# Performance work log

Hardware: AMD Instinct MI355X
Metric: run time of the kernel (lower is better)

Reference implementation:

```python
import jax, jax.numpy as jnp
import numpy as np

L, HID, H, D = 2, 128, 8, 16  # layers, hidden, heads, head_dim
N, E = 50000, 800000
CLAMP = 5.0
BN_SCALE = 1.0 / np.sqrt(1.0 + 1e-5)  # eval BN with running mean 0, var 1


def signed_sqrt(s):
    # sqrt(relu(s)) - sqrt(relu(-s)), with safe gradients at 0
    pos = jnp.sqrt(jnp.where(s > 0, s, 1.0))
    neg = jnp.sqrt(jnp.where(s < 0, -s, 1.0))
    return jnp.where(s > 0, pos, 0.0) - jnp.where(s < 0, neg, 0.0)


def setup_inputs() -> dict:
    key = jax.random.key(0)
    ks = jax.random.split(key, 32)
    sc = 0.05
    inp = {
        "x": jax.random.normal(ks[0], (N, HID), jnp.float32),
        "edge_index": jax.random.randint(ks[1], (2, E), 0, N, jnp.int64)
        if jax.config.jax_enable_x64 else jax.random.randint(ks[1], (2, E), 0, N, jnp.int32),
        "edge_attr": jax.random.normal(ks[2], (E, HID), jnp.float32),
        "Wq": jax.random.normal(ks[3], (L, HID, HID), jnp.float32) * sc,
        "bq": jnp.zeros((L, HID), jnp.float32),
        "Wk": jax.random.normal(ks[4], (L, HID, HID), jnp.float32) * sc,
        "Wv": jax.random.normal(ks[5], (L, HID, HID), jnp.float32) * sc,
        "We": jax.random.normal(ks[6], (L, HID, 2 * HID), jnp.float32) * sc,
        "be": jnp.zeros((L, 2 * HID), jnp.float32),
        "Aw": jax.random.normal(ks[7], (L, D, H, 1), jnp.float32) * 0.2,
        "VeRow": jax.random.normal(ks[8], (L, D, H, D), jnp.float32) * sc,
        "Woh": jax.random.normal(ks[9], (L, HID, HID), jnp.float32) * sc,
        "boh": jnp.zeros((L, HID), jnp.float32),
        "Woe": jax.random.normal(ks[10], (L, HID, HID), jnp.float32) * sc,
        "boe": jnp.zeros((L, HID), jnp.float32),
        "deg_coef": jax.random.normal(ks[11], (L, 1, HID, 2), jnp.float32) * 0.2,
        "W1": jax.random.normal(ks[12], (L, HID, 2 * HID), jnp.float32) * sc,
        "b1": jnp.zeros((L, 2 * HID), jnp.float32),
        "W2": jax.random.normal(ks[13], (L, 2 * HID, HID), jnp.float32) * sc,
        "b2": jnp.zeros((L, HID), jnp.float32),
    }
    return inp


def _forward(x, edge_attr, edge_index, Wq, bq, Wk, Wv, We, be, Aw, VeRow,
             Woh, boh, Woe, boe, deg_coef, W1, b1, W2, b2):
    src, dst = edge_index[0], edge_index[1]
    n = x.shape[0]
    deg = jax.ops.segment_sum(jnp.ones_like(dst, jnp.float32), dst, num_segments=n)
    log_deg = jnp.log(deg + 1.0)[:, None]  # [N,1]

    for l in range(L):
        Qh = (x @ Wq[l] + bq[l]).reshape(n, H, D)
        Kh = (x @ Wk[l]).reshape(n, H, D)
        Vh = (x @ Wv[l]).reshape(n, H, D)
        Ep = (edge_attr @ We[l] + be[l]).reshape(-1, H, 2 * D)
        E_w, E_b = Ep[:, :, :D], Ep[:, :, D:]

        s = (Kh[src] + Qh[dst]) * E_w           # [E,H,D]
        s = signed_sqrt(s) + E_b
        e_t = jax.nn.relu(s)                     # [E,H,D]
        wE = e_t.reshape(-1, H * D)

        sc = jnp.einsum('ehd,dhc->ehc', e_t, Aw[l])   # [E,H,1]
        sc = jnp.clip(sc, -CLAMP, CLAMP)
        m = jax.ops.segment_max(sc, dst, num_segments=n)
        a = jnp.exp(sc - m[dst])
        denom = jax.ops.segment_sum(a, dst, num_segments=n)[dst] + 1e-16
        attn = a / denom                          # [E,H,1]

        wV = jax.ops.segment_sum(Vh[src] * attn, dst, num_segments=n)   # [N,H,D]
        rowV = jax.ops.segment_sum(e_t * attn, dst, num_segments=n)     # [N,H,D]
        wV = wV + jnp.einsum('nhd,dhc->nhc', rowV, VeRow[l])

        h = wV.reshape(n, H * D)
        h = h * deg_coef[l, :, :, 0] + (h * log_deg) * deg_coef[l, :, :, 1]
        h = h @ Woh[l] + boh[l]
        e = wE @ Woe[l] + boe[l]
        h = (x + h) * BN_SCALE
        e = (edge_attr + e) * BN_SCALE
        h2 = jax.nn.relu(h @ W1[l] + b1[l]) @ W2[l] + b2[l]
        h = (h + h2) * BN_SCALE
        x, edge_attr = h, e
    return x, edge_attr


def reference(x, edge_index, edge_attr, Wq, bq, Wk, Wv, We, be, Aw, VeRow,
              Woh, boh, Woe, boe, deg_coef, W1, b1, W2, b2):
    return _forward(x, edge_attr, edge_index, Wq, bq, Wk, Wv, We, be, Aw, VeRow,
                    Woh, boh, Woe, boe, deg_coef, W1, b1, W2, b2)
```

## Files before the change

kernel.cpp:

```cpp
#include <hip/hip_runtime.h>

#define NN 50000
#define NE 800000
#define CLAMPV 5.0f
#define BNS 0.9999950000374997f
#define EPKS 132
#define NBLK 49

typedef __attribute__((ext_vector_type(8))) short s16x8;
typedef __attribute__((ext_vector_type(8))) __bf16 bf16x8;
typedef __attribute__((ext_vector_type(4))) float f32x4;

__device__ inline f32x4 mfma16(s16x8 a, s16x8 b, f32x4 c) {
    return __builtin_amdgcn_mfma_f32_16x16x32_bf16(
        __builtin_bit_cast(bf16x8, a), __builtin_bit_cast(bf16x8, b), c, 0, 0, 0);
}

__device__ inline unsigned short bf16r(float f) {
    return __builtin_bit_cast(unsigned short, (__bf16)f);
}

__device__ inline int pk2(float a, float b) {
    return (int)(unsigned)bf16r(a) | ((int)(unsigned)bf16r(b) << 16);
}

__device__ inline float b2f(unsigned short u) {
    return __builtin_bit_cast(float, (unsigned)u << 16);
}


__global__ __launch_bounds__(256) void k_deg(const int* __restrict__ ei, int* __restrict__ deg) {
    int e = blockIdx.x * 256 + threadIdx.x;
    if (e < NE) atomicAdd(&deg[ei[NE + e]], 1);
}

__global__ __launch_bounds__(1024) void k_scan1(const int* __restrict__ deg, int* __restrict__ offs,
                                                int* __restrict__ bsum, float* __restrict__ logdeg) {
    __shared__ int sm[1024];
    int i = blockIdx.x * 1024 + threadIdx.x;
    int v = (i < NN) ? deg[i] : 0;
    if (i < NN) logdeg[i] = logf((float)v + 1.0f);
    sm[threadIdx.x] = v;
    __syncthreads();
    for (int s = 1; s < 1024; s <<= 1) {
        int t = (threadIdx.x >= s) ? sm[threadIdx.x - s] : 0;
        __syncthreads();
        sm[threadIdx.x] += t;
        __syncthreads();
    }
    if (i < NN) offs[i + 1] = sm[threadIdx.x];
    if (threadIdx.x == 1023) bsum[blockIdx.x] = sm[1023];
    if (blockIdx.x == 0 && threadIdx.x == 0) offs[0] = 0;
}

__global__ void k_scan2(int* __restrict__ bsum) {
    if (threadIdx.x == 0) {
        int acc = 0;
        for (int i = 0; i < NBLK; ++i) { int v = bsum[i]; bsum[i] = acc; acc += v; }
    }
}

__global__ __launch_bounds__(1024) void k_scan3(int* __restrict__ offs, const int* __restrict__ bsum) {
    int i = blockIdx.x * 1024 + threadIdx.x;
    if (i < NN) offs[i + 1] += bsum[blockIdx.x];
}

__global__ __launch_bounds__(256) void k_fill(const int* __restrict__ ei, const int* __restrict__ offs,
                                              int* __restrict__ cursor, int* __restrict__ csr_src,
                                              int* __restrict__ epos) {
    int e = blockIdx.x * 256 + threadIdx.x;
    if (e < NE) {
        int d = ei[NE + e];
        int pos = offs[d] + atomicAdd(&cursor[d], 1);
        csr_src[pos] = ei[e];
        epos[e] = pos;
    }
}

#define PL_A (128*256)
#define PL_B (128*128)
__global__ __launch_bounds__(256) void k_packAll(
    const float* __restrict__ We,  const float* __restrict__ Woe, const float* __restrict__ Wq,
    const float* __restrict__ Wk,  const float* __restrict__ Wv,  const float* __restrict__ Woh,
    const float* __restrict__ W1,  const float* __restrict__ W2,  const float* __restrict__ VR,
    short* __restrict__ Wep,  short* __restrict__ Woep, short* __restrict__ Wqp,
    short* __restrict__ Wkp,  short* __restrict__ Wvp,  short* __restrict__ Wohp,
    short* __restrict__ W1p,  short* __restrict__ W2p,  short* __restrict__ VRp) {
    int s = blockIdx.x * 256 + threadIdx.x;
    const float* W; short* out; int ncol, perL; bool vr = false;
    if (s < 2 * PL_A) { W = We; out = Wep; ncol = 256; perL = PL_A; }
    else if ((s -= 2 * PL_A) < 2 * PL_B) { W = Woe; out = Woep; ncol = 128; perL = PL_B; }
    else if ((s -= 2 * PL_B) < 2 * PL_B) { W = Wq;  out = Wqp;  ncol = 128; perL = PL_B; }
    else if ((s -= 2 * PL_B) < 2 * PL_B) { W = Wk;  out = Wkp;  ncol = 128; perL = PL_B; }
    else if ((s -= 2 * PL_B) < 2 * PL_B) { W = Wv;  out = Wvp;  ncol = 128; perL = PL_B; }
    else if ((s -= 2 * PL_B) < 2 * PL_B) { W = Woh; out = Wohp; ncol = 128; perL = PL_B; }
    else if ((s -= 2 * PL_B) < 2 * PL_A) { W = W1;  out = W1p;  ncol = 256; perL = PL_A; }
    else if ((s -= 2 * PL_A) < 2 * PL_A) { W = W2;  out = W2p;  ncol = 128; perL = PL_A; }
    else if ((s -= 2 * PL_A) < 2 * PL_B) { W = VR;  out = VRp;  ncol = 128; perL = PL_B; vr = true; }
    else return;
    int l = s / perL, q = s % perL;
    int j = q & 7; int t2 = q >> 3; int kg = t2 & 3; t2 >>= 2;
    int col = t2 % ncol; int kt = t2 / ncol;
    int k = kt * 32 + kg * 8 + j;
    float v;
    if (vr) v = ((k >> 4) == (col >> 4)) ? VR[l * 2048 + (k & 15) * 128 + col] : 0.f;
    else    v = W[(size_t)l * perL + k * ncol + col];
    out[(size_t)l * perL + q] = (short)bf16r(v);
}


__global__ __launch_bounds__(512) void k_qkv(const float* __restrict__ x,
                                             const short* __restrict__ Wqp, const float* __restrict__ bq,
                                             const short* __restrict__ Wkp, const short* __restrict__ Wvp,
                                             unsigned short* __restrict__ Qh, unsigned short* __restrict__ Kh,
                                             unsigned short* __restrict__ Vh) {
    __shared__ short xsw[64 * 128];
    int t = threadIdx.x;
    int ci = t & 15, r0 = t >> 4;
    int n0 = blockIdx.x * 64;
    for (int rr = r0; rr < 64; rr += 32) {
        int n = n0 + rr;
        int4 pkv = make_int4(0, 0, 0, 0);
        if (n < NN) {
            const float4* src = (const float4*)(x + (size_t)n * 128 + ci * 8);
            float4 v0 = src[0], v1 = src[1];
            pkv.x = pk2(v0.x, v0.y); pkv.y = pk2(v0.z, v0.w);
            pkv.z = pk2(v1.x, v1.y); pkv.w = pk2(v1.z, v1.w);
        }
        int byte = (rr * 256 + ci * 16) ^ ((rr & 7) << 4);
        *(int4*)((char*)xsw + byte) = pkv;
    }
    __syncthreads();
    int lane = t & 63, w = t >> 6;
    int l15 = lane & 15, kg = lane >> 4;
    f32x4 acc[4][3];
#pragma unroll
    for (int m = 0; m < 4; ++m)
#pragma unroll
        for (int q = 0; q < 3; ++q) { acc[m][q][0] = 0.f; acc[m][q][1] = 0.f; acc[m][q][2] = 0.f; acc[m][q][3] = 0.f; }
    int col = w * 16 + l15;
#pragma unroll
    for (int kt = 0; kt < 4; ++kt) {
        s16x8 a[4];
#pragma unroll
        for (int m = 0; m < 4; ++m) {
            int row = m * 16 + l15;
            int abyte = (row * 256 + kt * 64 + kg * 16) ^ ((l15 & 7) << 4);
            a[m] = *(const s16x8*)((const char*)xsw + abyte);
        }
        size_t bo = ((size_t)((kt * 128 + col) * 4 + kg)) * 8;
        s16x8 bqf = *(const s16x8*)(Wqp + bo);
        s16x8 bkf = *(const s16x8*)(Wkp + bo);
        s16x8 bvf = *(const s16x8*)(Wvp + bo);
#pragma unroll
        for (int m = 0; m < 4; ++m) {
            acc[m][0] = mfma16(a[m], bqf, acc[m][0]);
            acc[m][1] = mfma16(a[m], bkf, acc[m][1]);
            acc[m][2] = mfma16(a[m], bvf, acc[m][2]);
        }
    }
    float bqv = bq[col];
#pragma unroll
    for (int m = 0; m < 4; ++m)
#pragma unroll
        for (int i = 0; i < 4; ++i) {
            int n = n0 + m * 16 + kg * 4 + i;
            if (n < NN) {
                Qh[(size_t)n * 128 + col] = bf16r(acc[m][0][i] + bqv);
                Kh[(size_t)n * 128 + col] = bf16r(acc[m][1][i]);
                Vh[(size_t)n * 128 + col] = bf16r(acc[m][2][i]);
            }
        }
}

template<bool IN_F32>
__global__ __launch_bounds__(512) void k_edgeA(const void* __restrict__ ea_, const int* __restrict__ ei,
                                               const int* __restrict__ epos,
                                               const short* __restrict__ Wep, const float* __restrict__ be,
                                               const float* __restrict__ Aw,
                                               const unsigned short* __restrict__ Qh,
                                               const unsigned short* __restrict__ Kh,
                                               unsigned short* __restrict__ e_t, float* __restrict__ sc,
                                               const short* __restrict__ Woep, const float* __restrict__ boe,
                                               void* __restrict__ eout_) {
    __shared__ short eas[64 * 128];
    __shared__ int epts[64 * EPKS];
    const float* eaf = (const float*)ea_;
    const unsigned short* eab = (const unsigned short*)ea_;
    unsigned short* eout_b = (unsigned short*)eout_;
    float* eout_f = (float*)eout_;

    int e0 = blockIdx.x * 64;
    int t = threadIdx.x;
    int ci = t & 15, r0 = t >> 4;
    int eA = e0 + r0, eB = eA + 32;
    int siA = ei[eA], diA = ei[NE + eA], posA = epos[eA];
    int siB = ei[eB], diB = ei[NE + eB], posB = epos[eB];

    {
#pragma unroll
        for (int h = 0; h < 2; ++h) {
            int rr = r0 + h * 32;
            int4 pkv;
            if (IN_F32) {
                const float4* src = (const float4*)(eaf + (size_t)(e0 + rr) * 128 + ci * 8);
                float4 v0 = src[0], v1 = src[1];
                pkv.x = pk2(v0.x, v0.y); pkv.y = pk2(v0.z, v0.w);
                pkv.z = pk2(v1.x, v1.y); pkv.w = pk2(v1.z, v1.w);
            } else {
                pkv = *(const int4*)(eab + (size_t)(e0 + rr) * 128 + ci * 8);
            }
            int byte = (rr * 256 + ci * 16) ^ ((rr & 7) << 4);
            *(int4*)((char*)eas + byte) = pkv;
        }
    }
    __syncthreads();
    union { int4 v; unsigned short us[8]; } kuA, quA, kuB, quB;
    kuA.v = *(const int4*)(Kh + (size_t)siA * 128 + ci * 8);
    quA.v = *(const int4*)(Qh + (size_t)diA * 128 + ci * 8);
    kuB.v = *(const int4*)(Kh + (size_t)siB * 128 + ci * 8);
    quB.v = *(const int4*)(Qh + (size_t)diB * 128 + ci * 8);

    int lane = t & 63, w = t >> 6;
    int l15 = lane & 15, kg = lane >> 4;
    {
        f32x4 acc[4][2];
#pragma unroll
        for (int m = 0; m < 4; ++m)
#pragma unroll
            for (int q = 0; q < 2; ++q) { acc[m][q][0] = 0.f; acc[m][q][1] = 0.f; acc[m][q][2] = 0.f; acc[m][q][3] = 0.f; }
#pragma unroll
        for (int kt = 0; kt < 4; ++kt) {
            s16x8 a[4];
#pragma unroll
            for (int m = 0; m < 4; ++m) {
                int row = m * 16 + l15;
                int abyte = (row * 256 + kt * 64 + kg * 16) ^ ((l15 & 7) << 4);
                a[m] = *(const s16x8*)((const char*)eas + abyte);
            }
#pragma unroll
            for (int q = 0; q < 2; ++q) {
                int col = w * 32 + q * 16 + l15;
                s16x8 b = *(const s16x8*)(Wep + ((size_t)((kt * 256 + col) * 4 + kg)) * 8);
#pragma unroll
                for (int m = 0; m < 4; ++m) acc[m][q] = mfma16(a[m], b, acc[m][q]);
            }
        }
        float bw = be[w * 32 + l15], bb = be[w * 32 + 16 + l15];
#pragma unroll
        for (int m = 0; m < 4; ++m)
#pragma unroll
            for (int i = 0; i < 4; ++i) {
                int row = m * 16 + kg * 4 + i;
                epts[row * EPKS + w * 16 + l15] = pk2(acc[m][0][i] + bw, acc[m][1][i] + bb);
            }
    }
    __syncthreads();
    int4 wA0, wA1, wB0, wB1;
    {
        const int4* pA = (const int4*)(epts + r0 * EPKS + ci * 8);
        wA0 = pA[0]; wA1 = pA[1];
        const int4* pB = (const int4*)(epts + (r0 + 32) * EPKS + ci * 8);
        wB0 = pB[0]; wB1 = pB[1];
    }
    __syncthreads();
    {
        int hh = ci >> 1, dbase = (ci & 1) * 8;
        float aw[8];
#pragma unroll
        for (int j = 0; j < 8; ++j) aw[j] = Aw[(dbase + j) * 8 + hh];
#pragma unroll
        for (int h = 0; h < 2; ++h) {
            int r = r0 + h * 32;
            int pos = h ? posB : posA;
            const unsigned short* kus = h ? kuB.us : kuA.us;
            const unsigned short* qus = h ? quB.us : quA.us;
            const int4 w0 = h ? wB0 : wA0;
            const int4 w1 = h ? wB1 : wA1;
            int prs[8] = {w0.x, w0.y, w0.z, w0.w, w1.x, w1.y, w1.z, w1.w};
            float p = 0.f;
            float etv[8];
#pragma unroll
            for (int j = 0; j < 8; ++j) {
                int pr = prs[j];
                float ew = b2f((unsigned short)pr);
                float ebv = b2f((unsigned short)((unsigned)pr >> 16));
                float kq = b2f(kus[j]) + b2f(qus[j]);
                float sv = kq * ew;
                float ss = copysignf(sqrtf(fabsf(sv)), sv);
                float et = fmaxf(ss + ebv, 0.f);
                etv[j] = et;
                p += et * aw[j];
            }
            int4 pkv;
            pkv.x = pk2(etv[0], etv[1]); pkv.y = pk2(etv[2], etv[3]);
            pkv.z = pk2(etv[4], etv[5]); pkv.w = pk2(etv[6], etv[7]);
            *(int4*)(e_t + (size_t)pos * 128 + ci * 8) = pkv;
            int byte = (r * 256 + ci * 16) ^ ((r & 7) << 4);
            *(int4*)((char*)epts + byte) = pkv;
            p += __shfl_xor(p, 1);
            if ((ci & 1) == 0) {
                float s = fminf(fmaxf(p, -CLAMPV), CLAMPV);
                sc[(size_t)pos * 8 + hh] = s;
            }
        }
    }
    __syncthreads();
    {
        f32x4 acc[4];
#pragma unroll
        for (int m = 0; m < 4; ++m) { acc[m][0] = 0.f; acc[m][1] = 0.f; acc[m][2] = 0.f; acc[m][3] = 0.f; }
        int col = w * 16 + l15;
#pragma unroll
        for (int kt = 0; kt < 4; ++kt) {
            s16x8 a[4];
#pragma unroll
            for (int m = 0; m < 4; ++m) {
                int row = m * 16 + l15;
                int abyte = (row * 256 + kt * 64 + kg * 16) ^ ((l15 & 7) << 4);
                a[m] = *(const s16x8*)((const char*)epts + abyte);
            }
            s16x8 b = *(const s16x8*)(Woep + ((size_t)((kt * 128 + col) * 4 + kg)) * 8);
#pragma unroll
            for (int m = 0; m < 4; ++m) acc[m] = mfma16(a[m], b, acc[m]);
        }
        float bb = boe[col];
#pragma unroll
        for (int m = 0; m < 4; ++m)
#pragma unroll
            for (int i = 0; i < 4; ++i) {
                int rr = m * 16 + kg * 4 + i;
                int rbyte = (rr * 256 + col * 2) ^ ((rr & 7) << 4);
                float res = b2f(*(const unsigned short*)((const char*)eas + rbyte));
                size_t idx = (size_t)(e0 + rr) * 128 + col;
                float v = (res + acc[m][i] + bb) * BNS;
                if (IN_F32) eout_b[idx] = bf16r(v);
                else        eout_f[idx] = v;
            }
    }
}

__global__ __launch_bounds__(64) void k_nattn(const int* __restrict__ offs, const int* __restrict__ csr_src,
                                              const float* __restrict__ sc,
                                              const unsigned short* __restrict__ e_t,
                                              const unsigned short* __restrict__ Vh,
                                              float* __restrict__ wV, float* __restrict__ rowV) {
    int n = blockIdx.x;
    int lane = threadIdx.x;
    int beg = offs[n], end = offs[n + 1];
    int h = lane & 7, es = lane >> 3;
    float m = -1e30f;
    for (int i = beg + es; i < end; i += 8)
        m = fmaxf(m, sc[(size_t)i * 8 + h]);
#pragma unroll
    for (int off = 8; off < 64; off <<= 1) m = fmaxf(m, __shfl_xor(m, off));
    float dsum = 0.0f;
    for (int i = beg + es; i < end; i += 8)
        dsum += expf(sc[(size_t)i * 8 + h] - m);
#pragma unroll
    for (int off = 8; off < 64; off <<= 1) dsum += __shfl_xor(dsum, off);
    float inv_d = 1.0f / (dsum + 1e-16f);

    int hv = lane >> 3;
    float mv = __shfl(m, hv);
    float idv = __shfl(inv_d, hv);
    float av0 = 0.0f, av1 = 0.0f, ar0 = 0.0f, ar1 = 0.0f;
    for (int i = beg; i < end; ++i) {
        float a = expf(sc[(size_t)i * 8 + hv] - mv) * idv;
        int s = csr_src[i];
        int v = ((const int*)Vh)[(size_t)s * 64 + lane];
        int u = ((const int*)e_t)[(size_t)i * 64 + lane];
        av0 += b2f((unsigned short)v) * a;
        av1 += b2f((unsigned short)((unsigned)v >> 16)) * a;
        ar0 += b2f((unsigned short)u) * a;
        ar1 += b2f((unsigned short)((unsigned)u >> 16)) * a;
    }
    *(float2*)(wV + (size_t)n * 128 + 2 * lane)   = make_float2(av0, av1);
    *(float2*)(rowV + (size_t)n * 128 + 2 * lane) = make_float2(ar0, ar1);
}

template<bool EMIT>
__global__ __launch_bounds__(256) void k_nodeB(
    const float* __restrict__ wV, const float* __restrict__ rowV,
    const short* __restrict__ VRp, const float* __restrict__ dc,
    const float* __restrict__ logdeg, const float* __restrict__ x,
    const short* __restrict__ Wohp, const float* __restrict__ boh,
    const short* __restrict__ W1p, const float* __restrict__ b1,
    const short* __restrict__ W2p, const float* __restrict__ b2,
    float* __restrict__ xout,
    const short* __restrict__ Wqp2, const float* __restrict__ bq2,
    const short* __restrict__ Wkp2, const short* __restrict__ Wvp2,
    unsigned short* __restrict__ Qh2, unsigned short* __restrict__ Kh2,
    unsigned short* __restrict__ Vh2) {
    __shared__ short bufA[32 * 128];
    __shared__ short bufU[32 * 256];
    int n0 = blockIdx.x * 32;
    int t = threadIdx.x;
    int ci = t & 15, r0 = t >> 4;
    {
#pragma unroll
        for (int h = 0; h < 2; ++h) {
            int rr = r0 + h * 16, n = n0 + rr;
            int4 pkv = make_int4(0, 0, 0, 0);
            if (n < NN) {
                const float4* src = (const float4*)(rowV + (size_t)n * 128 + ci * 8);
                float4 v0 = src[0], v1 = src[1];
                pkv.x = pk2(v0.x, v0.y); pkv.y = pk2(v0.z, v0.w);
                pkv.z = pk2(v1.x, v1.y); pkv.w = pk2(v1.z, v1.w);
            }
            int byte = (rr * 256 + ci * 16) ^ ((rr & 7) << 4);
            *(int4*)((char*)bufA + byte) = pkv;
        }
    }
    __syncthreads();
    int lane = t & 63, w = t >> 6;
    int l15 = lane & 15, kg = lane >> 4;
    int cq[2] = {w * 32 + l15, w * 32 + 16 + l15};
    {
        f32x4 acc[2][2];
#pragma unroll
        for (int m = 0; m < 2; ++m)
#pragma unroll
            for (int q = 0; q < 2; ++q)
#pragma unroll
                for (int i = 0; i < 4; ++i) {
                    int n = n0 + m * 16 + kg * 4 + i;
                    acc[m][q][i] = (n < NN) ? wV[(size_t)n * 128 + cq[q]] : 0.f;
                }
#pragma unroll
        for (int kt = 0; kt < 4; ++kt) {
            s16x8 a[2];
#pragma unroll
            for (int m = 0; m < 2; ++m) {
                int row = m * 16 + l15;
                int abyte = (row * 256 + kt * 64 + kg * 16) ^ ((l15 & 7) << 4);
                a[m] = *(const s16x8*)((const char*)bufA + abyte);
            }
#pragma unroll
            for (int q = 0; q < 2; ++q) {
                s16x8 b = *(const s16x8*)(VRp + ((size_t)((kt * 128 + cq[q]) * 4 + kg)) * 8);
#pragma unroll
                for (int m = 0; m < 2; ++m) acc[m][q] = mfma16(a[m], b, acc[m][q]);
            }
        }
#pragma unroll
        for (int q = 0; q < 2; ++q) {
            float d0 = dc[cq[q] * 2], d1 = dc[cq[q] * 2 + 1];
#pragma unroll
            for (int m = 0; m < 2; ++m)
#pragma unroll
                for (int i = 0; i < 4; ++i) {
                    int rr = m * 16 + kg * 4 + i, n = n0 + rr;
                    float ld = (n < NN) ? logdeg[n] : 0.f;
                    float hs = acc[m][q][i] * (d0 + ld * d1);
                    int byte = (rr * 256 + cq[q] * 2) ^ ((rr & 7) << 4);
                    *(unsigned short*)((char*)bufU + byte) = bf16r(hs);
                }
        }
    }
    __syncthreads();
    float h1r[2][2][4];
    {
        f32x4 acc[2][2];
#pragma unroll
        for (int m = 0; m < 2; ++m)
#pragma unroll
            for (int q = 0; q < 2; ++q) { acc[m][q][0] = 0.f; acc[m][q][1] = 0.f; acc[m][q][2] = 0.f; acc[m][q][3] = 0.f; }
#pragma unroll
        for (int kt = 0; kt < 4; ++kt) {
            s16x8 a[2];
#pragma unroll
            for (int m = 0; m < 2; ++m) {
                int row = m * 16 + l15;
                int abyte = (row * 256 + kt * 64 + kg * 16) ^ ((l15 & 7) << 4);
                a[m] = *(const s16x8*)((const char*)bufU + abyte);
            }
#pragma unroll
            for (int q = 0; q < 2; ++q) {
                s16x8 b = *(const s16x8*)(Wohp + ((size_t)((kt * 128 + cq[q]) * 4 + kg)) * 8);
#pragma unroll
                for (int m = 0; m < 2; ++m) acc[m][q] = mfma16(a[m], b, acc[m][q]);
            }
        }
#pragma unroll
        for (int q = 0; q < 2; ++q) {
            float bb = boh[cq[q]];
#pragma unroll
            for (int m = 0; m < 2; ++m)
#pragma unroll
                for (int i = 0; i < 4; ++i) {
                    int rr = m * 16 + kg * 4 + i, n = n0 + rr;
                    float xv = (n < NN) ? x[(size_t)n * 128 + cq[q]] : 0.f;
                    float h1 = (xv + acc[m][q][i] + bb) * BNS;
                    h1r[m][q][i] = h1;
                    int byte = (rr * 256 + cq[q] * 2) ^ ((rr & 7) << 4);
                    *(unsigned short*)((char*)bufA + byte) = bf16r(h1);
                }
        }
    }
    __syncthreads();
    {
        f32x4 acc[2][4];
#pragma unroll
        for (int m = 0; m < 2; ++m)
#pragma unroll
            for (int q = 0; q < 4; ++q) { acc[m][q][0] = 0.f; acc[m][q][1] = 0.f; acc[m][q][2] = 0.f; acc[m][q][3] = 0.f; }
#pragma unroll
        for (int kt = 0; kt < 4; ++kt) {
            s16x8 a[2];
#pragma unroll
            for (int m = 0; m < 2; ++m) {
                int row = m * 16 + l15;
                int abyte = (row * 256 + kt * 64 + kg * 16) ^ ((l15 & 7) << 4);
                a[m] = *(const s16x8*)((const char*)bufA + abyte);
            }
#pragma unroll
            for (int q = 0; q < 4; ++q) {
                int colq = w * 64 + q * 16 + l15;
                s16x8 b = *(const s16x8*)(W1p + ((size_t)((kt * 256 + colq) * 4 + kg)) * 8);
#pragma unroll
                for (int m = 0; m < 2; ++m) acc[m][q] = mfma16(a[m], b, acc[m][q]);
            }
        }
        __syncthreads();
#pragma unroll
        for (int q = 0; q < 4; ++q) {
            int colq = w * 64 + q * 16 + l15;
            float bb = b1[colq];
#pragma unroll
            for (int m = 0; m < 2; ++m)
#pragma unroll
                for (int i = 0; i < 4; ++i) {
                    int rr = m * 16 + kg * 4 + i;
                    float us = fmaxf(acc[m][q][i] + bb, 0.f);
                    int byte = (rr * 512 + colq * 2) ^ ((rr & 7) << 4);
                    *(unsigned short*)((char*)bufU + byte) = bf16r(us);
                }
        }
    }
    __syncthreads();
    {
        f32x4 acc[2][2];
#pragma unroll
        for (int m = 0; m < 2; ++m)
#pragma unroll
            for (int q = 0; q < 2; ++q) { acc[m][q][0] = 0.f; acc[m][q][1] = 0.f; acc[m][q][2] = 0.f; acc[m][q][3] = 0.f; }
#pragma unroll
        for (int kt = 0; kt < 8; ++kt) {
            s16x8 a[2];
#pragma unroll
            for (int m = 0; m < 2; ++m) {
                int row = m * 16 + l15;
                int abyte = (row * 512 + kt * 64 + kg * 16) ^ ((l15 & 7) << 4);
                a[m] = *(const s16x8*)((const char*)bufU + abyte);
            }
#pragma unroll
            for (int q = 0; q < 2; ++q) {
                s16x8 b = *(const s16x8*)(W2p + ((size_t)((kt * 128 + cq[q]) * 4 + kg)) * 8);
#pragma unroll
                for (int m = 0; m < 2; ++m) acc[m][q] = mfma16(a[m], b, acc[m][q]);
            }
        }
#pragma unroll
        for (int q = 0; q < 2; ++q) {
            float bb = b2[cq[q]];
#pragma unroll
            for (int m = 0; m < 2; ++m)
#pragma unroll
                for (int i = 0; i < 4; ++i) {
                    int rr = m * 16 + kg * 4 + i, n = n0 + rr;
                    float outv = (h1r[m][q][i] + acc[m][q][i] + bb) * BNS;
                    if (n < NN) xout[(size_t)n * 128 + cq[q]] = outv;
                    if (EMIT) {
                        int byte = (rr * 256 + cq[q] * 2) ^ ((rr & 7) << 4);
                        *(unsigned short*)((char*)bufA + byte) = bf16r(outv);
                    }
                }
        }
    }
    if (EMIT) {
        __syncthreads();
        f32x4 acc[2][2][3];
#pragma unroll
        for (int m = 0; m < 2; ++m)
#pragma unroll
            for (int q = 0; q < 2; ++q)
#pragma unroll
                for (int o = 0; o < 3; ++o) { acc[m][q][o][0] = 0.f; acc[m][q][o][1] = 0.f; acc[m][q][o][2] = 0.f; acc[m][q][o][3] = 0.f; }
#pragma unroll
        for (int kt = 0; kt < 4; ++kt) {
            s16x8 a[2];
#pragma unroll
            for (int m = 0; m < 2; ++m) {
                int row = m * 16 + l15;
                int abyte = (row * 256 + kt * 64 + kg * 16) ^ ((l15 & 7) << 4);
                a[m] = *(const s16x8*)((const char*)bufA + abyte);
            }
#pragma unroll
            for (int q = 0; q < 2; ++q) {
                size_t bo = ((size_t)((kt * 128 + cq[q]) * 4 + kg)) * 8;
                s16x8 bqf = *(const s16x8*)(Wqp2 + bo);
                s16x8 bkf = *(const s16x8*)(Wkp2 + bo);
                s16x8 bvf = *(const s16x8*)(Wvp2 + bo);
#pragma unroll
                for (int m = 0; m < 2; ++m) {
                    acc[m][q][0] = mfma16(a[m], bqf, acc[m][q][0]);
                    acc[m][q][1] = mfma16(a[m], bkf, acc[m][q][1]);
                    acc[m][q][2] = mfma16(a[m], bvf, acc[m][q][2]);
                }
            }
        }
#pragma unroll
        for (int q = 0; q < 2; ++q) {
            float bqv = bq2[cq[q]];
#pragma unroll
            for (int m = 0; m < 2; ++m)
#pragma unroll
                for (int i = 0; i < 4; ++i) {
                    int n = n0 + m * 16 + kg * 4 + i;
                    if (n < NN) {
                        Qh2[(size_t)n * 128 + cq[q]] = bf16r(acc[m][q][0][i] + bqv);
                        Kh2[(size_t)n * 128 + cq[q]] = bf16r(acc[m][q][1][i]);
                        Vh2[(size_t)n * 128 + cq[q]] = bf16r(acc[m][q][2][i]);
                    }
                }
        }
    }
}


extern "C" void kernel_launch(void* const* d_in, const int* in_sizes, int n_in,
                              void* d_out, int out_size, void* d_ws, size_t ws_size,
                              hipStream_t stream) {
    (void)in_sizes; (void)n_in; (void)out_size; (void)ws_size;
    const float* x_in0  = (const float*)d_in[0];
    const int*   ei     = (const int*)d_in[1];
    const float* ea_in0 = (const float*)d_in[2];
    const float* Wq = (const float*)d_in[3];
    const float* bq = (const float*)d_in[4];
    const float* Wk = (const float*)d_in[5];
    const float* Wv = (const float*)d_in[6];
    const float* We = (const float*)d_in[7];
    const float* be = (const float*)d_in[8];
    const float* Aw = (const float*)d_in[9];
    const float* VeRow = (const float*)d_in[10];
    const float* Woh = (const float*)d_in[11];
    const float* boh = (const float*)d_in[12];
    const float* Woe = (const float*)d_in[13];
    const float* boe = (const float*)d_in[14];
    const float* dc  = (const float*)d_in[15];
    const float* W1 = (const float*)d_in[16];
    const float* b1 = (const float*)d_in[17];
    const float* W2 = (const float*)d_in[18];
    const float* b2 = (const float*)d_in[19];

    char* ws = (char*)d_ws;
    size_t off = 0;
    auto alloc = [&](size_t bytes) { void* p = ws + off; off = (off + bytes + 255) & ~(size_t)255; return p; };
    int*   deg    = (int*)alloc((size_t)NN * 4);
    int*   cursor = (int*)alloc((size_t)NN * 4);
    int*   offs   = (int*)alloc((size_t)(NN + 1) * 4);
    int*   bsum   = (int*)alloc((size_t)64 * 4);
    int*   csr_src= (int*)alloc((size_t)NE * 4);
    int*   epos   = (int*)alloc((size_t)NE * 4);
    float* logdeg = (float*)alloc((size_t)NN * 4);
    unsigned short* Qh  = (unsigned short*)alloc((size_t)NN * 128 * 2);
    unsigned short* Kh  = (unsigned short*)alloc((size_t)NN * 128 * 2);
    unsigned short* Vh  = (unsigned short*)alloc((size_t)NN * 128 * 2);
    unsigned short* Qh2 = (unsigned short*)alloc((size_t)NN * 128 * 2);
    unsigned short* Kh2 = (unsigned short*)alloc((size_t)NN * 128 * 2);
    unsigned short* Vh2 = (unsigned short*)alloc((size_t)NN * 128 * 2);
    unsigned short* e_t = (unsigned short*)alloc((size_t)NE * 128 * 2);
    unsigned short* ea_bf = (unsigned short*)alloc((size_t)NE * 128 * 2);
    float* sc     = (float*)alloc((size_t)NE * 8 * 4);
    float* wV     = (float*)alloc((size_t)NN * 128 * 4);
    float* rowV   = (float*)alloc((size_t)NN * 128 * 4);
    short* Wep    = (short*)alloc((size_t)2 * 128 * 256 * 2);
    short* Woep   = (short*)alloc((size_t)2 * 128 * 128 * 2);
    short* Wqp    = (short*)alloc((size_t)2 * 128 * 128 * 2);
    short* Wkp    = (short*)alloc((size_t)2 * 128 * 128 * 2);
    short* Wvp    = (short*)alloc((size_t)2 * 128 * 128 * 2);
    short* Wohp   = (short*)alloc((size_t)2 * 128 * 128 * 2);
    short* W1p    = (short*)alloc((size_t)2 * 128 * 256 * 2);
    short* W2p    = (short*)alloc((size_t)2 * 256 * 128 * 2);
    short* VRp    = (short*)alloc((size_t)2 * 128 * 128 * 2);

    float* out_x = (float*)d_out;
    float* out_e = out_x + (size_t)NN * 128;

    hipError_t err;
    err = hipMemsetAsync(deg, 0, (size_t)NN * 4, stream); (void)err;
    err = hipMemsetAsync(cursor, 0, (size_t)NN * 4, stream); (void)err;

    k_deg<<<(NE + 255) / 256, 256, 0, stream>>>(ei, deg);
    k_scan1<<<NBLK, 1024, 0, stream>>>(deg, offs, bsum, logdeg);
    k_scan2<<<1, 64, 0, stream>>>(bsum);
    k_scan3<<<NBLK, 1024, 0, stream>>>(offs, bsum);
    k_fill<<<(NE + 255) / 256, 256, 0, stream>>>(ei, offs, cursor, csr_src, epos);
    k_packAll<<<1536, 256, 0, stream>>>(We, Woe, Wq, Wk, Wv, Woh, W1, W2, VeRow,
                                        Wep, Woep, Wqp, Wkp, Wvp, Wohp, W1p, W2p, VRp);

    k_qkv<<<(NN + 63) / 64, 512, 0, stream>>>(x_in0, Wqp, bq, Wkp, Wvp, Qh, Kh, Vh);
    k_edgeA<true><<<NE / 64, 512, 0, stream>>>(ea_in0, ei, epos, Wep, be, Aw, Qh, Kh,
                                               e_t, sc, Woep, boe, ea_bf);
    k_nattn<<<NN, 64, 0, stream>>>(offs, csr_src, sc, e_t, Vh, wV, rowV);
    k_nodeB<true><<<(NN + 31) / 32, 256, 0, stream>>>(
        wV, rowV, VRp, dc, logdeg, x_in0,
        Wohp, boh, W1p, b1, W2p, b2, out_x,
        Wqp + 128 * 128, bq + 128, Wkp + 128 * 128, Wvp + 128 * 128, Qh2, Kh2, Vh2);

    k_edgeA<false><<<NE / 64, 512, 0, stream>>>(ea_bf, ei, epos, Wep + 128 * 256, be + 256,
                                                Aw + 128, Qh2, Kh2, e_t, sc,
                                                Woep + 128 * 128, boe + 128, out_e);
    k_nattn<<<NN, 64, 0, stream>>>(offs, csr_src, sc, e_t, Vh2, wV, rowV);
    k_nodeB<false><<<(NN + 31) / 32, 256, 0, stream>>>(
        wV, rowV, VRp + 128 * 128, dc + 256, logdeg, out_x,
        Wohp + 128 * 128, boh + 128, W1p + 128 * 256, b1 + 256, W2p + 256 * 128, b2 + 128, out_x,
        nullptr, nullptr, nullptr, nullptr, nullptr, nullptr, nullptr);
}
```

Before: 1.035 ms.

## Store edge features in fp8, node aggregates in bf16, fuse softmax pass

The per-edge e_t intermediate is now stored as fp8 instead of bf16, which halves the largest intermediate write and gather in edgeA and nattn. The node-attention kernel drops its separate denominator pass, accumulating unnormalized sums and dividing at the end, and it writes wV and rowV as bf16 rather than fp32. The scan2 kernel is merged into scan3, where each block serially sums its prefix. The cost is lower precision in the e_t aggregation, which may hurt accuracy against the reference.

```diff
diff --git a/kernel.cpp b/kernel.cpp
--- a/kernel.cpp
+++ b/kernel.cpp
@@ -53,16 +53,16 @@
     if (blockIdx.x == 0 && threadIdx.x == 0) offs[0] = 0;
 }
 
-__global__ void k_scan2(int* __restrict__ bsum) {
+__global__ __launch_bounds__(1024) void k_scan3(int* __restrict__ offs, const int* __restrict__ bsum) {
+    __shared__ int pre;
     if (threadIdx.x == 0) {
         int acc = 0;
-        for (int i = 0; i < NBLK; ++i) { int v = bsum[i]; bsum[i] = acc; acc += v; }
-    }
-}
-
-__global__ __launch_bounds__(1024) void k_scan3(int* __restrict__ offs, const int* __restrict__ bsum) {
+        for (int i = 0; i < (int)blockIdx.x; ++i) acc += bsum[i];
+        pre = acc;
+    }
+    __syncthreads();
     int i = blockIdx.x * 1024 + threadIdx.x;
-    if (i < NN) offs[i + 1] += bsum[blockIdx.x];
+    if (i < NN) offs[i + 1] += pre;
 }
 
 __global__ __launch_bounds__(256) void k_fill(const int* __restrict__ ei, const int* __restrict__ offs,
@@ -180,7 +180,7 @@
                                                const float* __restrict__ Aw,
                                                const unsigned short* __restrict__ Qh,
                                                const unsigned short* __restrict__ Kh,
-                                               unsigned short* __restrict__ e_t, float* __restrict__ sc,
+                                               unsigned char* __restrict__ e8, float* __restrict__ sc,
                                                const short* __restrict__ Woep, const float* __restrict__ boe,
                                                void* __restrict__ eout_) {
     __shared__ short eas[64 * 128];
@@ -292,10 +292,14 @@
                 etv[j] = et;
                 p += et * aw[j];
             }
+            int lo = __builtin_amdgcn_cvt_pk_fp8_f32(etv[0], etv[1], 0, 0);
+            lo = __builtin_amdgcn_cvt_pk_fp8_f32(etv[2], etv[3], lo, 1);
+            int hi = __builtin_amdgcn_cvt_pk_fp8_f32(etv[4], etv[5], 0, 0);
+            hi = __builtin_amdgcn_cvt_pk_fp8_f32(etv[6], etv[7], hi, 1);
+            *(int2*)(e8 + (size_t)pos * 128 + ci * 8) = make_int2(lo, hi);
             int4 pkv;
             pkv.x = pk2(etv[0], etv[1]); pkv.y = pk2(etv[2], etv[3]);
             pkv.z = pk2(etv[4], etv[5]); pkv.w = pk2(etv[6], etv[7]);
-            *(int4*)(e_t + (size_t)pos * 128 + ci * 8) = pkv;
             int byte = (r * 256 + ci * 16) ^ ((r & 7) << 4);
             *(int4*)((char*)epts + byte) = pkv;
             p += __shfl_xor(p, 1);
@@ -342,9 +346,10 @@
 
 __global__ __launch_bounds__(64) void k_nattn(const int* __restrict__ offs, const int* __restrict__ csr_src,
                                               const float* __restrict__ sc,
-                                              const unsigned short* __restrict__ e_t,
+                                              const unsigned char* __restrict__ e8,
                                               const unsigned short* __restrict__ Vh,
-                                              float* __restrict__ wV, float* __restrict__ rowV) {
+                                              unsigned short* __restrict__ wVb,
+                                              unsigned short* __restrict__ rowVb) {
     int n = blockIdx.x;
     int lane = threadIdx.x;
     int beg = offs[n], end = offs[n + 1];
@@ -354,34 +359,28 @@
         m = fmaxf(m, sc[(size_t)i * 8 + h]);
 #pragma unroll
     for (int off = 8; off < 64; off <<= 1) m = fmaxf(m, __shfl_xor(m, off));
-    float dsum = 0.0f;
-    for (int i = beg + es; i < end; i += 8)
-        dsum += expf(sc[(size_t)i * 8 + h] - m);
-#pragma unroll
-    for (int off = 8; off < 64; off <<= 1) dsum += __shfl_xor(dsum, off);
-    float inv_d = 1.0f / (dsum + 1e-16f);
-
     int hv = lane >> 3;
     float mv = __shfl(m, hv);
-    float idv = __shfl(inv_d, hv);
-    float av0 = 0.0f, av1 = 0.0f, ar0 = 0.0f, ar1 = 0.0f;
+    float dsum = 0.f, av0 = 0.f, av1 = 0.f, ar0 = 0.f, ar1 = 0.f;
     for (int i = beg; i < end; ++i) {
-        float a = expf(sc[(size_t)i * 8 + hv] - mv) * idv;
+        float a = expf(sc[(size_t)i * 8 + hv] - mv);
+        dsum += a;
         int s = csr_src[i];
         int v = ((const int*)Vh)[(size_t)s * 64 + lane];
-        int u = ((const int*)e_t)[(size_t)i * 64 + lane];
+        int u8 = ((const unsigned short*)e8)[(size_t)i * 64 + lane];
         av0 += b2f((unsigned short)v) * a;
         av1 += b2f((unsigned short)((unsigned)v >> 16)) * a;
-        ar0 += b2f((unsigned short)u) * a;
-        ar1 += b2f((unsigned short)((unsigned)u >> 16)) * a;
-    }
-    *(float2*)(wV + (size_t)n * 128 + 2 * lane)   = make_float2(av0, av1);
-    *(float2*)(rowV + (size_t)n * 128 + 2 * lane) = make_float2(ar0, ar1);
+        ar0 += __builtin_amdgcn_cvt_f32_fp8(u8, 0) * a;
+        ar1 += __builtin_amdgcn_cvt_f32_fp8(u8, 1) * a;
+    }
+    float inv = 1.f / (dsum + 1e-16f);
+    ((int*)wVb)[(size_t)n * 64 + lane]   = pk2(av0 * inv, av1 * inv);
+    ((int*)rowVb)[(size_t)n * 64 + lane] = pk2(ar0 * inv, ar1 * inv);
 }
 
 template<bool EMIT>
 __global__ __launch_bounds__(256) void k_nodeB(
-    const float* __restrict__ wV, const float* __restrict__ rowV,
+    const unsigned short* __restrict__ wVb, const unsigned short* __restrict__ rowVb,
     const short* __restrict__ VRp, const float* __restrict__ dc,
     const float* __restrict__ logdeg, const float* __restrict__ x,
     const short* __restrict__ Wohp, const float* __restrict__ boh,
@@ -402,12 +401,7 @@
         for (int h = 0; h < 2; ++h) {
             int rr = r0 + h * 16, n = n0 + rr;
             int4 pkv = make_int4(0, 0, 0, 0);
-            if (n < NN) {
-                const float4* src = (const float4*)(rowV + (size_t)n * 128 + ci * 8);
-                float4 v0 = src[0], v1 = src[1];
-                pkv.x = pk2(v0.x, v0.y); pkv.y = pk2(v0.z, v0.w);
-                pkv.z = pk2(v1.x, v1.y); pkv.w = pk2(v1.z, v1.w);
-            }
+            if (n < NN) pkv = *(const int4*)(rowVb + (size_t)n * 128 + ci * 8);
             int byte = (rr * 256 + ci * 16) ^ ((rr & 7) << 4);
             *(int4*)((char*)bufA + byte) = pkv;
         }
@@ -425,7 +419,7 @@
 #pragma unroll
                 for (int i = 0; i < 4; ++i) {
                     int n = n0 + m * 16 + kg * 4 + i;
-                    acc[m][q][i] = (n < NN) ? wV[(size_t)n * 128 + cq[q]] : 0.f;
+                    acc[m][q][i] = (n < NN) ? b2f(wVb[(size_t)n * 128 + cq[q]]) : 0.f;
                 }
 #pragma unroll
         for (int kt = 0; kt < 4; ++kt) {
@@ -670,11 +664,11 @@
     unsigned short* Qh2 = (unsigned short*)alloc((size_t)NN * 128 * 2);
     unsigned short* Kh2 = (unsigned short*)alloc((size_t)NN * 128 * 2);
     unsigned short* Vh2 = (unsigned short*)alloc((size_t)NN * 128 * 2);
-    unsigned short* e_t = (unsigned short*)alloc((size_t)NE * 128 * 2);
+    unsigned char* e8   = (unsigned char*)alloc((size_t)NE * 128);
     unsigned short* ea_bf = (unsigned short*)alloc((size_t)NE * 128 * 2);
     float* sc     = (float*)alloc((size_t)NE * 8 * 4);
-    float* wV     = (float*)alloc((size_t)NN * 128 * 4);
-    float* rowV   = (float*)alloc((size_t)NN * 128 * 4);
+    unsigned short* wVb   = (unsigned short*)alloc((size_t)NN * 128 * 2);
+    unsigned short* rowVb = (unsigned short*)alloc((size_t)NN * 128 * 2);
     short* Wep    = (short*)alloc((size_t)2 * 128 * 256 * 2);
     short* Woep   = (short*)alloc((size_t)2 * 128 * 128 * 2);
     short* Wqp    = (short*)alloc((size_t)2 * 128 * 128 * 2);
@@ -694,7 +688,6 @@
 
     k_deg<<<(NE + 255) / 256, 256, 0, stream>>>(ei, deg);
     k_scan1<<<NBLK, 1024, 0, stream>>>(deg, offs, bsum, logdeg);
-    k_scan2<<<1, 64, 0, stream>>>(bsum);
     k_scan3<<<NBLK, 1024, 0, stream>>>(offs, bsum);
     k_fill<<<(NE + 255) / 256, 256, 0, stream>>>(ei, offs, cursor, csr_src, epos);
     k_packAll<<<1536, 256, 0, stream>>>(We, Woe, Wq, Wk, Wv, Woh, W1, W2, VeRow,
@@ -702,19 +695,19 @@
 
     k_qkv<<<(NN + 63) / 64, 512, 0, stream>>>(x_in0, Wqp, bq, Wkp, Wvp, Qh, Kh, Vh);
     k_edgeA<true><<<NE / 64, 512, 0, stream>>>(ea_in0, ei, epos, Wep, be, Aw, Qh, Kh,
-                                               e_t, sc, Woep, boe, ea_bf);
-    k_nattn<<<NN, 64, 0, stream>>>(offs, csr_src, sc, e_t, Vh, wV, rowV);
+                                               e8, sc, Woep, boe, ea_bf);
+    k_nattn<<<NN, 64, 0, stream>>>(offs, csr_src, sc, e8, Vh, wVb, rowVb);
     k_nodeB<true><<<(NN + 31) / 32, 256, 0, stream>>>(
-        wV, rowV, VRp, dc, logdeg, x_in0,
+        wVb, rowVb, VRp, dc, logdeg, x_in0,
         Wohp, boh, W1p, b1, W2p, b2, out_x,
         Wqp + 128 * 128, bq + 128, Wkp + 128 * 128, Wvp + 128 * 128, Qh2, Kh2, Vh2);
 
     k_edgeA<false><<<NE / 64, 512, 0, stream>>>(ea_bf, ei, epos, Wep + 128 * 256, be + 256,
-                                                Aw + 128, Qh2, Kh2, e_t, sc,
+                                                Aw + 128, Qh2, Kh2, e8, sc,
                                                 Woep + 128 * 128, boe + 128, out_e);
-    k_nattn<<<NN, 64, 0, stream>>>(offs, csr_src, sc, e_t, Vh2, wV, rowV);
+    k_nattn<<<NN, 64, 0, stream>>>(offs, csr_src, sc, e8, Vh2, wVb, rowVb);
     k_nodeB<false><<<(NN + 31) / 32, 256, 0, stream>>>(
-        wV, rowV, VRp + 128 * 128, dc + 256, logdeg, out_x,
+        wVb, rowVb, VRp + 128 * 128, dc + 256, logdeg, out_x,
         Wohp + 128 * 128, boh + 128, W1p + 128 * 256, b1 + 256, W2p + 256 * 128, b2 + 128, out_x,
         nullptr, nullptr, nullptr, nullptr, nullptr, nullptr, nullptr);
 }
```

Measured after the change: 967.1 us. 1.07x faster.
